# Kernel tuning notes

Measured on AMD Instinct MI355X. Metric: run time of the kernel, lower is better.

The kernel has to match this reference:

```python
import math
import jax, jax.numpy as jnp
import numpy as np

B, N, M = 8, 2048, 1024
INPUT_SIZE = 512
HEAD_DIM = 64
NUM_HEADS = 6
ATTN_SIZE = HEAD_DIM * NUM_HEADS
MAX_CLASSES = 512


def setup_inputs() -> dict:
    key = jax.random.key(0)
    k1, k2, k3, k4, k5, k6, k7 = jax.random.split(key, 7)
    bound = 1.0 / math.sqrt(INPUT_SIZE)
    return {
        "train_embeddings": jax.random.normal(k1, (B, N, INPUT_SIZE), jnp.float32),
        "test_embeddings": jax.random.normal(k2, (B, M, INPUT_SIZE), jnp.float32),
        "targets": jax.random.randint(k3, (B, N), 0, MAX_CLASSES),
        # torch nn.Linear weights, stored as [in, out] for direct matmul
        "Wq": jax.random.uniform(k4, (INPUT_SIZE, ATTN_SIZE), jnp.float32, -bound, bound),
        "bq": jax.random.uniform(k5, (ATTN_SIZE,), jnp.float32, -bound, bound),
        "Wk": jax.random.uniform(k6, (INPUT_SIZE, ATTN_SIZE), jnp.float32, -bound, bound),
        "bk": jax.random.uniform(k7, (ATTN_SIZE,), jnp.float32, -bound, bound),
    }


def reference(train_embeddings, test_embeddings, targets, Wq, bq, Wk, bk):
    b, m, _ = test_embeddings.shape
    # projections -> [B, S, H, D]
    q_bmhd = (test_embeddings @ Wq + bq).reshape(b, m, NUM_HEADS, HEAD_DIM)
    k_bnhd = (train_embeddings @ Wk + bk).reshape(b, -1, NUM_HEADS, HEAD_DIM)
    scale = 1.0 / math.sqrt(HEAD_DIM)  # SDPA default scale
    # attention scores [B, H, M, N]
    scores = jnp.einsum("bmhd,bnhd->bhmn", q_bmhd, k_bnhd) * scale
    attn = jax.nn.softmax(scores, axis=-1)
    # one-hot train targets [B, N, C]; chunk-folding in the torch code is a
    # memory trick — mathematically it is just attn @ one_hot per head
    onehot_bnc = jax.nn.one_hot(targets, MAX_CLASSES, dtype=q_bmhd.dtype)
    out_bhmc = jnp.einsum("bhmn,bnc->bhmc", attn, onehot_bnc)
    out_bmc = out_bhmc.mean(axis=1)          # mean over heads
    out_mbc = out_bmc.transpose(1, 0, 2)      # [M, B, C]
    return jnp.log(jnp.clip(out_mbc, 1e-05) + 3e-05)
```

## Files before the change

### kernel.cpp

```cpp
#include <hip/hip_runtime.h>
#include <hip/hip_bf16.h>

#define BQ 8
#define NN 2048
#define MM 1024
#define EE 512
#define NH 6
#define AA 384
#define CC 512

#define KROW_B (AA * 2)
#define TILE_B (16 * KROW_B)
#define STILE_B (32 * KROW_B)
#define WROW_B (EE * 2)
#define WTILE_B (16 * WROW_B)

#define QSCALE 0.1803368801111204f

typedef __bf16 bf16x8 __attribute__((ext_vector_type(8)));
typedef float  f32x4  __attribute__((ext_vector_type(4)));
using bf16 = __hip_bfloat16;

static __device__ __forceinline__ f32x4 mfma16(bf16x8 a, bf16x8 b, f32x4 c) {
  return __builtin_amdgcn_mfma_f32_16x16x32_bf16(a, b, c, 0, 0, 0);
}

typedef __attribute__((address_space(1))) const void gconst_void;
typedef __attribute__((address_space(3))) void lds_void_t;
static __device__ __forceinline__ void ld_lds16(const void* g, void* l) {
  __builtin_amdgcn_global_load_lds((gconst_void*)g, (lds_void_t*)l, 16, 0, 0);
}

static __device__ __forceinline__ unsigned short f2bfu(float x) {
  union { __hip_bfloat16 h; unsigned short u; } v;
  v.h = __float2bfloat16(x);
  return v.u;
}
static __device__ __forceinline__ float bf2f(unsigned short u) {
  union { unsigned int i; float f; } x;
  x.i = ((unsigned int)u) << 16;
  return x.f;
}

__global__ __launch_bounds__(256) void transw_kernel(
    const float* __restrict__ Wq, const float* __restrict__ Wk,
    bf16* __restrict__ WqT, bf16* __restrict__ WkT) {
  __shared__ float t[64][65];
  int id = blockIdx.x;
  const float* W = (id < 48) ? Wq : Wk;
  bf16* WT = (id < 48) ? WqT : WkT;
  if (id >= 48) id -= 48;
  int kb = (id / 6) * 64, nb = (id % 6) * 64;
  int tid = threadIdx.x;
  int lr = tid >> 4, lc = (tid & 15) * 4;
  #pragma unroll
  for (int p = 0; p < 4; p++) {
    int k = lr + p * 16;
    float4 v = *reinterpret_cast<const float4*>(W + (size_t)(kb + k) * AA + nb + lc);
    t[k][lc] = v.x; t[k][lc + 1] = v.y; t[k][lc + 2] = v.z; t[k][lc + 3] = v.w;
  }
  __syncthreads();
  #pragma unroll
  for (int p = 0; p < 4; p++) {
    int n = lr + p * 16;
    bf16* dst = WT + (size_t)(nb + n) * EE + kb + lc;
    dst[0] = __float2bfloat16(t[lc][n]);
    dst[1] = __float2bfloat16(t[lc + 1][n]);
    dst[2] = __float2bfloat16(t[lc + 2][n]);
    dst[3] = __float2bfloat16(t[lc + 3][n]);
  }
}

__global__ __launch_bounds__(512) void build_kernel(const int* __restrict__ targets,
                                                    int* __restrict__ offs, int* __restrict__ idxs) {
  __shared__ int cnt[CC], ssum[CC], pos[CC];
  int b = blockIdx.x, tid = threadIdx.x;
  cnt[tid] = 0;
  __syncthreads();
  int t[4];
  #pragma unroll
  for (int i = 0; i < 4; i++) {
    t[i] = targets[b * NN + tid * 4 + i];
    atomicAdd(&cnt[t[i]], 1);
  }
  __syncthreads();
  ssum[tid] = cnt[tid];
  __syncthreads();
  for (int d = 1; d < CC; d <<= 1) {
    int v = (tid >= d) ? ssum[tid - d] : 0;
    __syncthreads();
    ssum[tid] += v;
    __syncthreads();
  }
  int excl = ssum[tid] - cnt[tid];
  offs[b * (CC + 1) + tid] = excl;
  if (tid == CC - 1) offs[b * (CC + 1) + CC] = NN;
  pos[tid] = excl;
  __syncthreads();
  #pragma unroll
  for (int i = 0; i < 4; i++) {
    int p = atomicAdd(&pos[t[i]], 1);
    idxs[b * NN + p] = tid * 4 + i;
  }
}

__global__ __launch_bounds__(256, 3) void proj_kernel(
    const float* __restrict__ test, const float* __restrict__ train,
    const bf16* __restrict__ WqT, const bf16* __restrict__ WkT,
    const float* __restrict__ bq, const float* __restrict__ bk,
    bf16* __restrict__ Qb, bf16* __restrict__ Kb)
{
  __shared__ char wbuf[3][WTILE_B];
  int tid = threadIdx.x, wid = tid >> 6, lane = tid & 63;
  int bid = blockIdx.x;
  int sub = bid & 1, unit = bid >> 1;
  const float* A; const bf16* WT; const float* bias; bf16* C; float scale; int m0;
  if (unit < 128) { A = test;  WT = WqT; bias = bq; C = Qb; scale = QSCALE; m0 = unit * 64; }
  else            { A = train; WT = WkT; bias = bk; C = Kb; scale = 1.0f;   m0 = (unit - 128) * 64; }
  m0 += wid * 16;
  int row = lane & 15, hi = lane >> 4;

  bf16x8 af[16];
  const float* arow = A + (size_t)(m0 + row) * EE + hi * 8;
  #pragma unroll
  for (int ks = 0; ks < 16; ks++) {
    float4 u = *reinterpret_cast<const float4*>(arow + ks * 32);
    float4 v = *reinterpret_cast<const float4*>(arow + ks * 32 + 4);
    bf16x8 f;
    f[0] = (__bf16)u.x; f[1] = (__bf16)u.y; f[2] = (__bf16)u.z; f[3] = (__bf16)u.w;
    f[4] = (__bf16)v.x; f[5] = (__bf16)v.y; f[6] = (__bf16)v.z; f[7] = (__bf16)v.w;
    af[ks] = f;
  }

  int ldso[4], srco[4];
  #pragma unroll
  for (int i = 0; i < 4; i++) {
    int off = tid * 16 + i * 4096;
    int rw = off >> 10, c = off & 1023;
    ldso[i] = off;
    srco[i] = rw * WROW_B + (c ^ ((rw & 7) << 4));
  }
  const char* wgbase = (const char*)WT + (size_t)sub * 12 * WTILE_B;
  int sw = (row & 7) << 4;

  auto stage = [&](int t, int buf) {
    const char* src = wgbase + (size_t)t * WTILE_B;
    #pragma unroll
    for (int i = 0; i < 4; i++) ld_lds16(src + srco[i], wbuf[buf] + ldso[i]);
  };
  auto compute = [&](int buf, int t) {
    const char* wb = wbuf[buf] + row * WROW_B;
    f32x4 acc0 = {0.f, 0.f, 0.f, 0.f}, acc1 = {0.f, 0.f, 0.f, 0.f};
    #pragma unroll
    for (int ks = 0; ks < 16; ks += 2) {
      bf16x8 w0 = *reinterpret_cast<const bf16x8*>(wb + ((hi * 16 + ks * 64) ^ sw));
      bf16x8 w1 = *reinterpret_cast<const bf16x8*>(wb + ((hi * 16 + (ks + 1) * 64) ^ sw));
      acc0 = mfma16(af[ks], w0, acc0);
      acc1 = mfma16(af[ks + 1], w1, acc1);
    }
    f32x4 acc = acc0 + acc1;
    int ocol = (sub * 12 + t) * 16 + row;
    float bv = bias[ocol];
    #pragma unroll
    for (int j = 0; j < 4; j++)
      C[(size_t)(m0 + hi * 4 + j) * AA + ocol] = __float2bfloat16((acc[j] + bv) * scale);
  };

  stage(0, 0);
  stage(1, 1);
  asm volatile("s_waitcnt vmcnt(4)" ::: "memory");
  __builtin_amdgcn_s_barrier();
  __builtin_amdgcn_sched_barrier(0);
  stage(2, 2);
  compute(0, 0);

  int cur = 1, stg = 0;
  #pragma unroll 1
  for (int t = 1; t < 11; t++) {
    asm volatile("s_waitcnt vmcnt(8)" ::: "memory");
    __builtin_amdgcn_s_barrier();
    __builtin_amdgcn_sched_barrier(0);
    if (t < 10) stage(t + 2, stg);
    compute(cur, t);
    cur = cur + 1 < 3 ? cur + 1 : 0;
    stg = stg + 1 < 3 ? stg + 1 : 0;
  }
  asm volatile("s_waitcnt vmcnt(4)" ::: "memory");
  __builtin_amdgcn_s_barrier();
  __builtin_amdgcn_sched_barrier(0);
  compute(cur, 11);
}

__global__ __launch_bounds__(256, 2) void zpass_kernel(
    const bf16* __restrict__ Qb, const bf16* __restrict__ Kb, float* __restrict__ Zp)
{
  __shared__ char kbuf[2][STILE_B];
  int id = blockIdx.x;
  int b = id & 7, r = id >> 3, mt = r & 7, nc = r >> 3;
  int tid = threadIdx.x, wid = tid >> 6, lane = tid & 63;
  int m0 = mt * 128 + wid * 32, n0 = nc * 256;
  int row = lane & 15, hi = lane >> 4;

  bf16x8 qf[2][12];
  #pragma unroll
  for (int s = 0; s < 2; s++) {
    const bf16* qrow = Qb + ((size_t)(b * MM + m0 + s * 16 + row)) * AA + hi * 8;
    #pragma unroll
    for (int ks = 0; ks < 12; ks++) qf[s][ks] = *reinterpret_cast<const bf16x8*>(qrow + ks * 32);
  }

  int ldso[6], srco[6];
  #pragma unroll
  for (int i = 0; i < 6; i++) {
    int off = tid * 16 + i * 4096;
    int rw = off / KROW_B, c = off - rw * KROW_B;
    ldso[i] = off;
    srco[i] = rw * KROW_B + (c ^ ((rw & 7) << 4));
  }
  const char* kgbase = (const char*)(Kb + ((size_t)(b * NN + n0)) * AA);

  int sw = (row & 7) << 4;
  int rbase = row * KROW_B;
  int x0 = rbase + ((hi * 16) ^ sw);
  int x1 = rbase + (((hi * 16) + 64) ^ sw);

  float zacc[2][NH][4];
  #pragma unroll
  for (int s = 0; s < 2; s++)
    #pragma unroll
    for (int h = 0; h < NH; h++)
      #pragma unroll
      for (int j = 0; j < 4; j++) zacc[s][h][j] = 0.f;

  auto stage = [&](int t, int buf) {
    const char* src = kgbase + (size_t)t * STILE_B;
    #pragma unroll
    for (int i = 0; i < 6; i++) ld_lds16(src + srco[i], kbuf[buf] + ldso[i]);
  };
  auto compute = [&](int buf) {
    __builtin_amdgcn_s_setprio(1);
    #pragma unroll
    for (int sub = 0; sub < 2; sub++) {
      const char* kb = kbuf[buf] + sub * TILE_B;
      #pragma unroll
      for (int h = 0; h < NH; h++) {
        bf16x8 k0 = *reinterpret_cast<const bf16x8*>(kb + h * 128 + x0);
        bf16x8 k1 = *reinterpret_cast<const bf16x8*>(kb + h * 128 + x1);
        f32x4 a0 = {0.f, 0.f, 0.f, 0.f}, a1 = {0.f, 0.f, 0.f, 0.f};
        a0 = mfma16(qf[0][2 * h], k0, a0);
        a1 = mfma16(qf[1][2 * h], k0, a1);
        a0 = mfma16(qf[0][2 * h + 1], k1, a0);
        a1 = mfma16(qf[1][2 * h + 1], k1, a1);
        #pragma unroll
        for (int j = 0; j < 4; j++) {
          zacc[0][h][j] += __builtin_amdgcn_exp2f(a0[j]);
          zacc[1][h][j] += __builtin_amdgcn_exp2f(a1[j]);
        }
      }
    }
    __builtin_amdgcn_s_setprio(0);
  };

  stage(0, 0);
  asm volatile("s_waitcnt vmcnt(0)" ::: "memory");
  __builtin_amdgcn_s_barrier();
  __builtin_amdgcn_sched_barrier(0);
  stage(1, 1);
  compute(0);

  #pragma unroll 1
  for (int i = 1; i < 8; i++) {
    asm volatile("s_waitcnt vmcnt(0)" ::: "memory");
    __builtin_amdgcn_s_barrier();
    __builtin_amdgcn_sched_barrier(0);
    if (i < 7) stage(i + 1, (i + 1) & 1);
    compute(i & 1);
  }

  #pragma unroll
  for (int s = 0; s < 2; s++)
    #pragma unroll
    for (int h = 0; h < NH; h++)
      #pragma unroll
      for (int j = 0; j < 4; j++) {
        float v = zacc[s][h][j];
        v += __shfl_xor(v, 1); v += __shfl_xor(v, 2);
        v += __shfl_xor(v, 4); v += __shfl_xor(v, 8);
        zacc[s][h][j] = v;
      }
  if (row == 0) {
    #pragma unroll
    for (int s = 0; s < 2; s++)
      #pragma unroll
      for (int h = 0; h < NH; h++)
        #pragma unroll
        for (int j = 0; j < 4; j++)
          Zp[(((size_t)nc * 8 + b) * NH + h) * MM + m0 + s * 16 + hi * 4 + j] = zacc[s][h][j];
  }
}

__global__ __launch_bounds__(256, 2) void wpass_kernel(
    const bf16* __restrict__ Qb, const bf16* __restrict__ Kb,
    const float* __restrict__ Zp, bf16* __restrict__ W2)
{
  __shared__ char kbuf[2][STILE_B];
  int id = blockIdx.x;
  int b = id & 7, r = id >> 3, mt = r & 7, nc = r >> 3;
  int tid = threadIdx.x, wid = tid >> 6, lane = tid & 63;
  int m0 = mt * 128 + wid * 32, n0 = nc * 256;
  int row = lane & 15, hi = lane >> 4;

  bf16x8 qf[2][12];
  #pragma unroll
  for (int s = 0; s < 2; s++) {
    const bf16* qrow = Qb + ((size_t)(b * MM + m0 + s * 16 + row)) * AA + hi * 8;
    #pragma unroll
    for (int ks = 0; ks < 12; ks++) qf[s][ks] = *reinterpret_cast<const bf16x8*>(qrow + ks * 32);
  }

  float rz[2][NH][4];
  #pragma unroll
  for (int s = 0; s < 2; s++)
    #pragma unroll
    for (int h = 0; h < NH; h++) {
      f32x4 z = {0.f, 0.f, 0.f, 0.f};
      #pragma unroll
      for (int p = 0; p < 8; p++)
        z += *reinterpret_cast<const f32x4*>(Zp + (((size_t)p * 8 + b) * NH + h) * MM + m0 + s * 16 + hi * 4);
      #pragma unroll
      for (int j = 0; j < 4; j++) rz[s][h][j] = 1.0f / (6.0f * z[j]);
    }

  int ldso[6], srco[6];
  #pragma unroll
  for (int i = 0; i < 6; i++) {
    int off = tid * 16 + i * 4096;
    int rw = off / KROW_B, c = off - rw * KROW_B;
    ldso[i] = off;
    srco[i] = rw * KROW_B + (c ^ ((rw & 7) << 4));
  }
  const char* kgbase = (const char*)(Kb + ((size_t)(b * NN + n0)) * AA);

  int sw = (row & 7) << 4;
  int rbase = row * KROW_B;
  int x0 = rbase + ((hi * 16) ^ sw);
  int x1 = rbase + (((hi * 16) + 64) ^ sw);

  int m4a = (m0 >> 2) + hi;
  int m4b = ((m0 + 16) >> 2) + hi;

  auto stage = [&](int t, int buf) {
    const char* src = kgbase + (size_t)t * STILE_B;
    #pragma unroll
    for (int i = 0; i < 6; i++) ld_lds16(src + srco[i], kbuf[buf] + ldso[i]);
  };
  auto compute = [&](int buf, int st) {
    #pragma unroll
    for (int sub = 0; sub < 2; sub++) {
      const char* kb = kbuf[buf] + sub * TILE_B;
      __builtin_amdgcn_s_setprio(1);
      float w0a = 0.f, w1a = 0.f, w2a = 0.f, w3a = 0.f;
      float w0b = 0.f, w1b = 0.f, w2b = 0.f, w3b = 0.f;
      #pragma unroll
      for (int h = 0; h < NH; h++) {
        bf16x8 k0 = *reinterpret_cast<const bf16x8*>(kb + h * 128 + x0);
        bf16x8 k1 = *reinterpret_cast<const bf16x8*>(kb + h * 128 + x1);
        f32x4 a0 = {0.f, 0.f, 0.f, 0.f}, a1 = {0.f, 0.f, 0.f, 0.f};
        a0 = mfma16(qf[0][2 * h], k0, a0);
        a1 = mfma16(qf[1][2 * h], k0, a1);
        a0 = mfma16(qf[0][2 * h + 1], k1, a0);
        a1 = mfma16(qf[1][2 * h + 1], k1, a1);
        w0a += __builtin_amdgcn_exp2f(a0[0]) * rz[0][h][0];
        w1a += __builtin_amdgcn_exp2f(a0[1]) * rz[0][h][1];
        w2a += __builtin_amdgcn_exp2f(a0[2]) * rz[0][h][2];
        w3a += __builtin_amdgcn_exp2f(a0[3]) * rz[0][h][3];
        w0b += __builtin_amdgcn_exp2f(a1[0]) * rz[1][h][0];
        w1b += __builtin_amdgcn_exp2f(a1[1]) * rz[1][h][1];
        w2b += __builtin_amdgcn_exp2f(a1[2]) * rz[1][h][2];
        w3b += __builtin_amdgcn_exp2f(a1[3]) * rz[1][h][3];
      }
      __builtin_amdgcn_s_setprio(0);
      int n = n0 + (st * 2 + sub) * 16 + row;
      ushort4 qa, qb2;
      qa.x = f2bfu(w0a); qa.y = f2bfu(w1a); qa.z = f2bfu(w2a); qa.w = f2bfu(w3a);
      qb2.x = f2bfu(w0b); qb2.y = f2bfu(w1b); qb2.z = f2bfu(w2b); qb2.w = f2bfu(w3b);
      *reinterpret_cast<ushort4*>((unsigned short*)W2 + (((size_t)(b * 256 + m4a)) * NN + n) * 4) = qa;
      *reinterpret_cast<ushort4*>((unsigned short*)W2 + (((size_t)(b * 256 + m4b)) * NN + n) * 4) = qb2;
    }
  };

  stage(0, 0);
  asm volatile("s_waitcnt vmcnt(0)" ::: "memory");
  __builtin_amdgcn_s_barrier();
  __builtin_amdgcn_sched_barrier(0);
  stage(1, 1);
  compute(0, 0);

  #pragma unroll 1
  for (int i = 1; i < 8; i++) {
    asm volatile("s_waitcnt vmcnt(4)" ::: "memory");
    __builtin_amdgcn_s_barrier();
    __builtin_amdgcn_sched_barrier(0);
    if (i < 7) stage(i + 1, (i + 1) & 1);
    compute(i & 1, i);
  }
}

__global__ __launch_bounds__(512) void gather_kernel(
    const bf16* __restrict__ W2, const int* __restrict__ offs,
    const int* __restrict__ idxs, float* __restrict__ out)
{
  __shared__ char wl[2 * NN * 8];
  __shared__ int ilb[NN];
  int id = blockIdx.x;
  int b = id & 7, mt = id >> 3;
  int g0 = mt * 2;
  int tid = threadIdx.x;

  const uint4* src = (const uint4*)((const unsigned short*)W2 + ((size_t)(b * 256 + g0)) * NN * 4);
  uint4* dst = (uint4*)wl;
  #pragma unroll
  for (int i = tid; i < 2 * NN * 8 / 16; i += 512) dst[i] = src[i];
  const int* il = idxs + b * NN;
  #pragma unroll
  for (int i = tid; i < NN; i += 512) ilb[i] = il[i];
  __syncthreads();

  int c = tid;
  int o0 = offs[b * (CC + 1) + c], o1 = offs[b * (CC + 1) + c + 1];
  #pragma unroll 1
  for (int g = 0; g < 2; g++) {
    float s0 = 0.f, s1 = 0.f, s2 = 0.f, s3 = 0.f;
    for (int i = o0; i < o1; i++) {
      int idx = ilb[i];
      ushort4 v = *reinterpret_cast<const ushort4*>(wl + g * (NN * 8) + idx * 8);
      s0 += bf2f(v.x); s1 += bf2f(v.y); s2 += bf2f(v.z); s3 += bf2f(v.w);
    }
    int m = mt * 8 + g * 4;
    out[((size_t)(m + 0) * BQ + b) * CC + c] = __logf(fmaxf(s0, 1e-5f) + 3e-5f);
    out[((size_t)(m + 1) * BQ + b) * CC + c] = __logf(fmaxf(s1, 1e-5f) + 3e-5f);
    out[((size_t)(m + 2) * BQ + b) * CC + c] = __logf(fmaxf(s2, 1e-5f) + 3e-5f);
    out[((size_t)(m + 3) * BQ + b) * CC + c] = __logf(fmaxf(s3, 1e-5f) + 3e-5f);
  }
}

extern "C" void kernel_launch(void* const* d_in, const int* in_sizes, int n_in,
                              void* d_out, int out_size, void* d_ws, size_t ws_size,
                              hipStream_t stream) {
  const float* train = (const float*)d_in[0];
  const float* test  = (const float*)d_in[1];
  const int*   tgt   = (const int*)d_in[2];
  const float* Wq    = (const float*)d_in[3];
  const float* bq    = (const float*)d_in[4];
  const float* Wk    = (const float*)d_in[5];
  const float* bk    = (const float*)d_in[6];
  float* out = (float*)d_out;

  char* ws = (char*)d_ws;
  bf16*  WqT  = (bf16*)(ws);
  bf16*  WkT  = (bf16*)(ws + 393216);
  bf16*  Qb   = (bf16*)(ws + 786432);
  bf16*  Kb   = (bf16*)(ws + 7077888);
  float* Zp   = (float*)(ws + 19660800);
  bf16*  Wbuf = (bf16*)(ws + 21233664);
  int*   offs = (int*)(ws + 54788096);
  int*   idxs = (int*)(ws + 54804512);

  transw_kernel<<<96, 256, 0, stream>>>(Wq, Wk, WqT, WkT);
  build_kernel<<<BQ, 512, 0, stream>>>(tgt, offs, idxs);
  proj_kernel<<<768, 256, 0, stream>>>(test, train, WqT, WkT, bq, bk, Qb, Kb);
  zpass_kernel<<<512, 256, 0, stream>>>(Qb, Kb, Zp);
  wpass_kernel<<<512, 256, 0, stream>>>(Qb, Kb, Zp, Wbuf);
  gather_kernel<<<1024, 512, 0, stream>>>(Wbuf, offs, idxs, out);
}
```

Measured before the change: 108.4 us.

## Sort K rows by class, fold softmax normalizer into MFMA, merge prep kernels

```diff
diff --git a/kernel.cpp b/kernel.cpp
--- a/kernel.cpp
+++ b/kernel.cpp
@@ -42,46 +42,49 @@
   return x.f;
 }
 
-__global__ __launch_bounds__(256) void transw_kernel(
+__global__ __launch_bounds__(512) void prep_kernel(
     const float* __restrict__ Wq, const float* __restrict__ Wk,
-    bf16* __restrict__ WqT, bf16* __restrict__ WkT) {
+    bf16* __restrict__ WqT, bf16* __restrict__ WkT,
+    const int* __restrict__ targets, int* __restrict__ offs, int* __restrict__ idxs)
+{
   __shared__ float t[64][65];
-  int id = blockIdx.x;
-  const float* W = (id < 48) ? Wq : Wk;
-  bf16* WT = (id < 48) ? WqT : WkT;
-  if (id >= 48) id -= 48;
-  int kb = (id / 6) * 64, nb = (id % 6) * 64;
-  int tid = threadIdx.x;
-  int lr = tid >> 4, lc = (tid & 15) * 4;
-  #pragma unroll
-  for (int p = 0; p < 4; p++) {
-    int k = lr + p * 16;
-    float4 v = *reinterpret_cast<const float4*>(W + (size_t)(kb + k) * AA + nb + lc);
-    t[k][lc] = v.x; t[k][lc + 1] = v.y; t[k][lc + 2] = v.z; t[k][lc + 3] = v.w;
-  }
-  __syncthreads();
-  #pragma unroll
-  for (int p = 0; p < 4; p++) {
-    int n = lr + p * 16;
-    bf16* dst = WT + (size_t)(nb + n) * EE + kb + lc;
-    dst[0] = __float2bfloat16(t[lc][n]);
-    dst[1] = __float2bfloat16(t[lc + 1][n]);
-    dst[2] = __float2bfloat16(t[lc + 2][n]);
-    dst[3] = __float2bfloat16(t[lc + 3][n]);
-  }
-}
-
-__global__ __launch_bounds__(512) void build_kernel(const int* __restrict__ targets,
-                                                    int* __restrict__ offs, int* __restrict__ idxs) {
   __shared__ int cnt[CC], ssum[CC], pos[CC];
-  int b = blockIdx.x, tid = threadIdx.x;
+  int bid = blockIdx.x, tid = threadIdx.x;
+  if (bid < 96) {
+    if (tid >= 256) { __syncthreads(); __syncthreads(); return; }
+    int id = bid;
+    const float* W = (id < 48) ? Wq : Wk;
+    bf16* WT = (id < 48) ? WqT : WkT;
+    if (id >= 48) id -= 48;
+    int kb = (id / 6) * 64, nb = (id % 6) * 64;
+    int lr = tid >> 4, lc = (tid & 15) * 4;
+    #pragma unroll
+    for (int p = 0; p < 4; p++) {
+      int k = lr + p * 16;
+      float4 v = *reinterpret_cast<const float4*>(W + (size_t)(kb + k) * AA + nb + lc);
+      t[k][lc] = v.x; t[k][lc + 1] = v.y; t[k][lc + 2] = v.z; t[k][lc + 3] = v.w;
+    }
+    __syncthreads();
+    #pragma unroll
+    for (int p = 0; p < 4; p++) {
+      int n = lr + p * 16;
+      bf16* dst = WT + (size_t)(nb + n) * EE + kb + lc;
+      dst[0] = __float2bfloat16(t[lc][n]);
+      dst[1] = __float2bfloat16(t[lc + 1][n]);
+      dst[2] = __float2bfloat16(t[lc + 2][n]);
+      dst[3] = __float2bfloat16(t[lc + 3][n]);
+    }
+    __syncthreads();
+    return;
+  }
+  int b = bid - 96;
   cnt[tid] = 0;
   __syncthreads();
-  int t[4];
+  int tv[4];
   #pragma unroll
   for (int i = 0; i < 4; i++) {
-    t[i] = targets[b * NN + tid * 4 + i];
-    atomicAdd(&cnt[t[i]], 1);
+    tv[i] = targets[b * NN + tid * 4 + i];
+    atomicAdd(&cnt[tv[i]], 1);
   }
   __syncthreads();
   ssum[tid] = cnt[tid];
@@ -99,7 +102,7 @@
   __syncthreads();
   #pragma unroll
   for (int i = 0; i < 4; i++) {
-    int p = atomicAdd(&pos[t[i]], 1);
+    int p = atomicAdd(&pos[tv[i]], 1);
     idxs[b * NN + p] = tid * 4 + i;
   }
 }
@@ -108,20 +111,30 @@
     const float* __restrict__ test, const float* __restrict__ train,
     const bf16* __restrict__ WqT, const bf16* __restrict__ WkT,
     const float* __restrict__ bq, const float* __restrict__ bk,
+    const int* __restrict__ idxs,
     bf16* __restrict__ Qb, bf16* __restrict__ Kb)
 {
   __shared__ char wbuf[3][WTILE_B];
   int tid = threadIdx.x, wid = tid >> 6, lane = tid & 63;
   int bid = blockIdx.x;
   int sub = bid & 1, unit = bid >> 1;
-  const float* A; const bf16* WT; const float* bias; bf16* C; float scale; int m0;
-  if (unit < 128) { A = test;  WT = WqT; bias = bq; C = Qb; scale = QSCALE; m0 = unit * 64; }
-  else            { A = train; WT = WkT; bias = bk; C = Kb; scale = 1.0f;   m0 = (unit - 128) * 64; }
-  m0 += wid * 16;
+  const bf16* WT; const float* bias; bf16* C; float scale; int m0;
+  const float* arow;
   int row = lane & 15, hi = lane >> 4;
+  if (unit < 128) {
+    WT = WqT; bias = bq; C = Qb; scale = QSCALE; m0 = unit * 64 + wid * 16;
+    arow = test + (size_t)(m0 + row) * EE + hi * 8;
+  } else {
+    WT = WkT; bias = bk; C = Kb; scale = 1.0f;
+    int g0 = (unit - 128) * 64 + wid * 16;
+    m0 = g0;
+    int g = g0 + row;
+    int b = g >> 11, pos = g & (NN - 1);
+    int srcrow = idxs[b * NN + pos];
+    arow = train + ((size_t)b * NN + srcrow) * EE + hi * 8;
+  }
 
   bf16x8 af[16];
-  const float* arow = A + (size_t)(m0 + row) * EE + hi * 8;
   #pragma unroll
   for (int ks = 0; ks < 16; ks++) {
     float4 u = *reinterpret_cast<const float4*>(arow + ks * 32);
@@ -318,7 +331,7 @@
     for (int ks = 0; ks < 12; ks++) qf[s][ks] = *reinterpret_cast<const bf16x8*>(qrow + ks * 32);
   }
 
-  float rz[2][NH][4];
+  f32x4 lrz4[2][NH];
   #pragma unroll
   for (int s = 0; s < 2; s++)
     #pragma unroll
@@ -327,8 +340,10 @@
       #pragma unroll
       for (int p = 0; p < 8; p++)
         z += *reinterpret_cast<const f32x4*>(Zp + (((size_t)p * 8 + b) * NH + h) * MM + m0 + s * 16 + hi * 4);
-      #pragma unroll
-      for (int j = 0; j < 4; j++) rz[s][h][j] = 1.0f / (6.0f * z[j]);
+      f32x4 l;
+      #pragma unroll
+      for (int j = 0; j < 4; j++) l[j] = -__log2f(6.0f * z[j]);
+      lrz4[s][h] = l;
     }
 
   int ldso[6], srco[6];
@@ -365,19 +380,18 @@
       for (int h = 0; h < NH; h++) {
         bf16x8 k0 = *reinterpret_cast<const bf16x8*>(kb + h * 128 + x0);
         bf16x8 k1 = *reinterpret_cast<const bf16x8*>(kb + h * 128 + x1);
-        f32x4 a0 = {0.f, 0.f, 0.f, 0.f}, a1 = {0.f, 0.f, 0.f, 0.f};
-        a0 = mfma16(qf[0][2 * h], k0, a0);
-        a1 = mfma16(qf[1][2 * h], k0, a1);
+        f32x4 a0 = mfma16(qf[0][2 * h], k0, lrz4[0][h]);
+        f32x4 a1 = mfma16(qf[1][2 * h], k0, lrz4[1][h]);
         a0 = mfma16(qf[0][2 * h + 1], k1, a0);
         a1 = mfma16(qf[1][2 * h + 1], k1, a1);
-        w0a += __builtin_amdgcn_exp2f(a0[0]) * rz[0][h][0];
-        w1a += __builtin_amdgcn_exp2f(a0[1]) * rz[0][h][1];
-        w2a += __builtin_amdgcn_exp2f(a0[2]) * rz[0][h][2];
-        w3a += __builtin_amdgcn_exp2f(a0[3]) * rz[0][h][3];
-        w0b += __builtin_amdgcn_exp2f(a1[0]) * rz[1][h][0];
-        w1b += __builtin_amdgcn_exp2f(a1[1]) * rz[1][h][1];
-        w2b += __builtin_amdgcn_exp2f(a1[2]) * rz[1][h][2];
-        w3b += __builtin_amdgcn_exp2f(a1[3]) * rz[1][h][3];
+        w0a += __builtin_amdgcn_exp2f(a0[0]);
+        w1a += __builtin_amdgcn_exp2f(a0[1]);
+        w2a += __builtin_amdgcn_exp2f(a0[2]);
+        w3a += __builtin_amdgcn_exp2f(a0[3]);
+        w0b += __builtin_amdgcn_exp2f(a1[0]);
+        w1b += __builtin_amdgcn_exp2f(a1[1]);
+        w2b += __builtin_amdgcn_exp2f(a1[2]);
+        w3b += __builtin_amdgcn_exp2f(a1[3]);
       }
       __builtin_amdgcn_s_setprio(0);
       int n = n0 + (st * 2 + sub) * 16 + row;
@@ -407,11 +421,9 @@
 }
 
 __global__ __launch_bounds__(512) void gather_kernel(
-    const bf16* __restrict__ W2, const int* __restrict__ offs,
-    const int* __restrict__ idxs, float* __restrict__ out)
+    const bf16* __restrict__ W2, const int* __restrict__ offs, float* __restrict__ out)
 {
   __shared__ char wl[2 * NN * 8];
-  __shared__ int ilb[NN];
   int id = blockIdx.x;
   int b = id & 7, mt = id >> 3;
   int g0 = mt * 2;
@@ -421,19 +433,17 @@
   uint4* dst = (uint4*)wl;
   #pragma unroll
   for (int i = tid; i < 2 * NN * 8 / 16; i += 512) dst[i] = src[i];
-  const int* il = idxs + b * NN;
-  #pragma unroll
-  for (int i = tid; i < NN; i += 512) ilb[i] = il[i];
   __syncthreads();
 
   int c = tid;
   int o0 = offs[b * (CC + 1) + c], o1 = offs[b * (CC + 1) + c + 1];
   #pragma unroll 1
   for (int g = 0; g < 2; g++) {
+    const char* base = wl + g * (NN * 8);
     float s0 = 0.f, s1 = 0.f, s2 = 0.f, s3 = 0.f;
+    #pragma unroll 1
     for (int i = o0; i < o1; i++) {
-      int idx = ilb[i];
-      ushort4 v = *reinterpret_cast<const ushort4*>(wl + g * (NN * 8) + idx * 8);
+      ushort4 v = *reinterpret_cast<const ushort4*>(base + (size_t)i * 8);
       s0 += bf2f(v.x); s1 += bf2f(v.y); s2 += bf2f(v.z); s3 += bf2f(v.w);
     }
     int m = mt * 8 + g * 4;
@@ -466,10 +476,9 @@
   int*   offs = (int*)(ws + 54788096);
   int*   idxs = (int*)(ws + 54804512);
 
-  transw_kernel<<<96, 256, 0, stream>>>(Wq, Wk, WqT, WkT);
-  build_kernel<<<BQ, 512, 0, stream>>>(tgt, offs, idxs);
-  proj_kernel<<<768, 256, 0, stream>>>(test, train, WqT, WkT, bq, bk, Qb, Kb);
+  prep_kernel<<<104, 512, 0, stream>>>(Wq, Wk, WqT, WkT, tgt, offs, idxs);
+  proj_kernel<<<768, 256, 0, stream>>>(test, train, WqT, WkT, bq, bk, idxs, Qb, Kb);
   zpass_kernel<<<512, 256, 0, stream>>>(Qb, Kb, Zp);
   wpass_kernel<<<512, 256, 0, stream>>>(Qb, Kb, Zp, Wbuf);
-  gather_kernel<<<1024, 512, 0, stream>>>(Wbuf, offs, idxs, out);
-}
+  gather_kernel<<<1024, 512, 0, stream>>>(Wbuf, offs, out);
+}
```

New measurement: 103.7 us. -4.4%, faster.
